# Performance work log

Hardware: AMD Instinct MI355X
Metric: run time of the kernel (lower is better)

## Reference

```python
import jax, jax.numpy as jnp
import numpy as np

NUM_CLASSES = 1000
MEM_SIZE = 200
FEAT_DIM = 512
BATCH = 512
TEMP = 0.07
MARGIN = 0.5
K_POS = 50   # memory positives per anchor (source: memory_positives[:50])
K_NEG = 20   # memory negatives per other class (source: [:20])


def _l2norm(x, axis=-1, eps=1e-12):
    n = jnp.sqrt(jnp.sum(x * x, axis=axis, keepdims=True))
    return x / jnp.maximum(n, eps)


def setup_inputs() -> dict:
    key = jax.random.key(0)
    k1, k2, k3 = jax.random.split(key, 3)
    features = jax.random.normal(k1, (BATCH, FEAT_DIM), dtype=jnp.float32)
    labels = jax.random.randint(k2, (BATCH,), 0, NUM_CLASSES, dtype=jnp.int32)
    memory_bank = jax.random.normal(k3, (NUM_CLASSES, MEM_SIZE, FEAT_DIM), dtype=jnp.float32)
    memory_bank = _l2norm(memory_bank, axis=2)  # buffer is normalized in __init__
    memory_ptr = jnp.zeros((NUM_CLASSES,), dtype=jnp.int32)
    return {"features": features, "labels": labels,
            "memory_bank": memory_bank, "memory_ptr": memory_ptr}


def reference(features, labels, memory_bank, memory_ptr):
    B, D = features.shape
    C, M, _ = memory_bank.shape

    f = _l2norm(features, axis=1)  # [B, D]

    # ---- memory-bank update (no_grad in torch): write each normalized feature
    # at ptr[label] + (rank of this sample among same-label samples in batch) ----
    onehot = jax.nn.one_hot(labels, C, dtype=jnp.int32)          # [B, C]
    cum = jnp.cumsum(onehot, axis=0)                              # [B, C]
    rank = cum[jnp.arange(B), labels] - 1                         # prior same-label count
    group_size = cum[-1][labels]                                  # occurrences of own label
    first_idx = jnp.argmax(onehot, axis=0)                        # first batch index per class
    write_pos = (memory_ptr[labels] + rank) % M
    mem = memory_bank.at[labels, write_pos].set(jax.lax.stop_gradient(f))
    mem = jax.lax.stop_gradient(mem)

    # ---- in-batch positives (faithful to the source's mask quirk:
    # positions compared against the FULL-batch first-occurrence index) ----
    S_batch = (f @ f.T) / TEMP                                    # [B, B]
    same = labels[:, None] == labels[None, :]
    batch_mask = same & (rank[None, :] != first_idx[labels][:, None]) & (group_size[:, None] > 1)
    pos_sum_batch = jnp.sum(jnp.where(batch_mask, S_batch, 0.0), axis=1)
    cnt_batch = jnp.sum(batch_mask, axis=1)

    # ---- memory similarities: only first K_POS slots are ever used ----
    S_mem = jnp.einsum('bd,ckd->bck', f, mem[:, :K_POS]) / TEMP   # [B, C, K_POS]

    # positives: own class, first K_POS slots
    own = S_mem[jnp.arange(B), labels]                            # [B, K_POS]
    pos_sum = pos_sum_batch + jnp.sum(own, axis=1)
    pos_cnt = (cnt_batch + K_POS).astype(f.dtype)
    pos_loss = -pos_sum / pos_cnt

    # negatives: all other classes, first K_NEG slots; hard-negative mean if any > margin
    sims_neg = S_mem[:, :, :K_NEG]                                # [B, C, K_NEG]
    cls_mask = (jnp.arange(C)[None, :] != labels[:, None])[:, :, None]
    hard = (sims_neg > MARGIN) & cls_mask
    hard_cnt = jnp.sum(hard, axis=(1, 2))
    hard_sum = jnp.sum(jnp.where(hard, sims_neg, 0.0), axis=(1, 2))
    all_sum = jnp.sum(jnp.where(cls_mask, sims_neg, 0.0), axis=(1, 2))
    all_cnt = jnp.asarray((C - 1) * K_NEG, dtype=f.dtype)
    neg_loss = jnp.where(hard_cnt > 0,
                         hard_sum / jnp.maximum(hard_cnt, 1).astype(f.dtype),
                         all_sum / all_cnt)

    return jnp.mean(pos_loss + neg_loss)
```

## Files before the change

kernel.cpp:

```cpp
#include <hip/hip_runtime.h>
#include <hip/hip_bf16.h>
#include <math.h>

#define BATCH 512
#define FEAT 512
#define NCLS 1000
#define MSZ 200
#define KP 50
#define KN 20
#define INV_TEMP (1.0f/0.07f)
#define MARGIN 0.5f
#define NBROWS 20032
#define NCB 313
#define NPART (NCB*2)

typedef __attribute__((ext_vector_type(8))) short short8;
typedef __attribute__((ext_vector_type(4))) float f32x4;

__device__ __forceinline__ unsigned short f2bf(float x) {
    __hip_bfloat16 h = __float2bfloat16(x);
    return *reinterpret_cast<unsigned short*>(&h);
}

__device__ __forceinline__ void gload_lds16(const void* g, void* l) {
    __builtin_amdgcn_global_load_lds(
        (const __attribute__((address_space(1))) void*)g,
        (__attribute__((address_space(3))) void*)l, 16, 0, 0);
}

__global__ void k_init(int* __restrict__ ov, float* __restrict__ own_sum) {
    int i = blockIdx.x * blockDim.x + threadIdx.x;
    if (i < NCLS * KP) ov[i] = -1;
    if (i < BATCH) own_sum[i] = 0.f;
}

__global__ void k_norm(const float* __restrict__ x, float* __restrict__ f,
                       unsigned short* __restrict__ fb) {
    int row = blockIdx.x;
    int t = threadIdx.x;
    float4 v = ((const float4*)(x + (size_t)row * FEAT))[t];
    float ss = v.x*v.x + v.y*v.y + v.z*v.z + v.w*v.w;
    for (int off = 32; off; off >>= 1) ss += __shfl_down(ss, off);
    __shared__ float w[2];
    if ((t & 63) == 0) w[t >> 6] = ss;
    __syncthreads();
    float inv = 1.f / fmaxf(sqrtf(w[0] + w[1]), 1e-12f);
    float4 o; o.x = v.x*inv; o.y = v.y*inv; o.z = v.z*inv; o.w = v.w*inv;
    ((float4*)(f + (size_t)row * FEAT))[t] = o;
    unsigned long long pk = (unsigned long long)f2bf(o.x)
                          | ((unsigned long long)f2bf(o.y) << 16)
                          | ((unsigned long long)f2bf(o.z) << 32)
                          | ((unsigned long long)f2bf(o.w) << 48);
    *(unsigned long long*)(fb + (size_t)row * FEAT + t * 4) = pk;
}

__global__ void k_meta(const int* __restrict__ labels, const int* __restrict__ mptr,
                       int* __restrict__ rank, int* __restrict__ gs,
                       int* __restrict__ fidx, int* __restrict__ ov) {
    __shared__ int lab[BATCH];
    int i = threadIdx.x;
    lab[i] = labels[i];
    __syncthreads();
    int l = lab[i];
    int r = 0, cnt = 0, first = -1;
    for (int j = 0; j < BATCH; j++) {
        if (lab[j] == l) { if (j < i) r++; cnt++; if (first < 0) first = j; }
    }
    rank[i] = r; gs[i] = cnt; fidx[i] = first;
    int wp = (mptr[l] + r) % MSZ;
    if (wp < KP) ov[l * KP + wp] = i;
}

__global__ __launch_bounds__(256) void k_conv(const float* __restrict__ f,
                                              const float* __restrict__ bank,
                                              const int* __restrict__ ov,
                                              unsigned short* __restrict__ Bm) {
    int g = blockIdx.x * 4 + (threadIdx.x >> 6);
    int lane = threadIdx.x & 63;
    unsigned short* dst = Bm + (size_t)g * FEAT + lane * 8;
    if (g >= NCLS * KN) {
        short8 z = {0,0,0,0,0,0,0,0};
        *(short8*)dst = z;
        return;
    }
    int c = g / KN, s = g - c * KN;
    int o = ov[c * KP + s];
    const float* src = (o >= 0) ? (f + (size_t)o * FEAT)
                                : (bank + ((size_t)c * MSZ + s) * FEAT);
    const float4* s4 = (const float4*)(src + lane * 8);
    float4 v0 = s4[0], v1 = s4[1];
    short8 out;
    out[0] = (short)f2bf(v0.x); out[1] = (short)f2bf(v0.y);
    out[2] = (short)f2bf(v0.z); out[3] = (short)f2bf(v0.w);
    out[4] = (short)f2bf(v1.x); out[5] = (short)f2bf(v1.y);
    out[6] = (short)f2bf(v1.z); out[7] = (short)f2bf(v1.w);
    *(short8*)dst = out;
}

__global__ void k_batchpos(const float* __restrict__ f, const int* __restrict__ labels,
                           const int* __restrict__ rank, const int* __restrict__ gs,
                           const int* __restrict__ fidx,
                           float* __restrict__ psb, float* __restrict__ cb) {
    int i = blockIdx.x;
    int t = threadIdx.x;
    __shared__ float fi[FEAT];
    for (int d = t; d < FEAT; d += 256) fi[d] = f[(size_t)i * FEAT + d];
    __syncthreads();
    int li = labels[i], fi_first = fidx[i], gsi = gs[i];
    float s = 0.f, c = 0.f;
    if (gsi > 1) {
        for (int j = t; j < BATCH; j += 256) {
            if (labels[j] == li && rank[j] != fi_first) {
                const float4* fj = (const float4*)(f + (size_t)j * FEAT);
                float acc = 0.f;
                #pragma unroll 8
                for (int d = 0; d < FEAT / 4; d++) {
                    float4 a = ((const float4*)fi)[d];
                    float4 b = fj[d];
                    acc += a.x*b.x + a.y*b.y + a.z*b.z + a.w*b.w;
                }
                s += acc * INV_TEMP;
                c += 1.f;
            }
        }
    }
    for (int off = 32; off; off >>= 1) { s += __shfl_down(s, off); c += __shfl_down(c, off); }
    __shared__ float ws[4], wc[4];
    if ((t & 63) == 0) { ws[t >> 6] = s; wc[t >> 6] = c; }
    __syncthreads();
    if (t == 0) {
        psb[i] = ws[0] + ws[1] + ws[2] + ws[3];
        cb[i]  = wc[0] + wc[1] + wc[2] + wc[3];
    }
}

#define BK 64
__global__ __launch_bounds__(256) void k_main(
    const unsigned short* __restrict__ fb, const unsigned short* __restrict__ Bm,
    const int* __restrict__ labels,
    float* __restrict__ own_sum,
    float* __restrict__ pa_all, float* __restrict__ pa_hs, float* __restrict__ pa_hc)
{
    int cb = blockIdx.y;
    int rbase = blockIdx.x * 128;
    int t = threadIdx.x;
    int w = t >> 6, lane = t & 63;
    int wr = w >> 1, wc = w & 1;
    int ln15 = lane & 15, quad = lane >> 4;

    __shared__ __align__(16) unsigned short As[128][BK];
    __shared__ __align__(16) unsigned short Bs[64][BK];

    f32x4 acc[4][2];
    #pragma unroll
    for (int i = 0; i < 4; i++)
        #pragma unroll
        for (int j = 0; j < 2; j++) acc[i][j] = (f32x4){0.f, 0.f, 0.f, 0.f};

    const char* aSrc[4]; void* aDst[4];
    const char* bSrc[2]; void* bDst[2];
    #pragma unroll
    for (int q = 0; q < 4; q++) {
        unsigned int L = q * 4096 + w * 1024 + lane * 16;
        int row = L >> 7;
        int part = L & 127;
        aSrc[q] = (const char*)fb + (size_t)(rbase + row) * (FEAT * 2) + part;
        aDst[q] = (char*)&As[0][0] + (q * 4096 + w * 1024);
    }
    #pragma unroll
    for (int q = 0; q < 2; q++) {
        unsigned int L = q * 4096 + w * 1024 + lane * 16;
        int row = L >> 7;
        int part = L & 127;
        bSrc[q] = (const char*)Bm + (size_t)(cb * 64 + row) * (FEAT * 2) + part;
        bDst[q] = (char*)&Bs[0][0] + (q * 4096 + w * 1024);
    }

    for (int k0 = 0; k0 < FEAT; k0 += BK) {
        __syncthreads();
        #pragma unroll
        for (int q = 0; q < 4; q++) gload_lds16(aSrc[q] + k0 * 2, aDst[q]);
        #pragma unroll
        for (int q = 0; q < 2; q++) gload_lds16(bSrc[q] + k0 * 2, bDst[q]);
        __syncthreads();

        #pragma unroll
        for (int kh = 0; kh < BK; kh += 32) {
            short8 a[4], b[2];
            #pragma unroll
            for (int i = 0; i < 4; i++)
                a[i] = *(const short8*)&As[wr * 64 + i * 16 + ln15][kh + quad * 8];
            #pragma unroll
            for (int j = 0; j < 2; j++)
                b[j] = *(const short8*)&Bs[wc * 32 + j * 16 + ln15][kh + quad * 8];
            #pragma unroll
            for (int i = 0; i < 4; i++)
                #pragma unroll
                for (int j = 0; j < 2; j++)
                    acc[i][j] = __builtin_amdgcn_mfma_f32_16x16x32_bf16(a[i], b[j], acc[i][j], 0, 0, 0);
        }
    }

    #pragma unroll
    for (int i = 0; i < 4; i++) {
        #pragma unroll
        for (int r = 0; r < 4; r++) {
            int grow = rbase + wr * 64 + i * 16 + quad * 4 + r;
            int lab = labels[grow];
            float own = 0.f, alls = 0.f, hs = 0.f, hc = 0.f;
            #pragma unroll
            for (int j = 0; j < 2; j++) {
                int gcol = cb * 64 + wc * 32 + j * 16 + ln15;
                float sim = acc[i][j][r] * INV_TEMP;
                if (gcol < NCLS * KN) {
                    int c = gcol / KN;
                    if (c == lab) {
                        own += sim;
                    } else {
                        alls += sim;
                        if (sim > MARGIN) { hs += sim; hc += 1.f; }
                    }
                }
            }
            #pragma unroll
            for (int off = 8; off; off >>= 1) {
                own  += __shfl_down(own,  off, 16);
                alls += __shfl_down(alls, off, 16);
                hs   += __shfl_down(hs,   off, 16);
                hc   += __shfl_down(hc,   off, 16);
            }
            if (ln15 == 0) {
                size_t pidx = (size_t)(cb * 2 + wc) * BATCH + grow;
                pa_all[pidx] = alls; pa_hs[pidx] = hs; pa_hc[pidx] = hc;
                if (own != 0.f) atomicAdd(&own_sum[grow], own);
            }
        }
    }
}

__global__ __launch_bounds__(256) void k_ownextra(
    const float* __restrict__ f, const float* __restrict__ bank,
    const int* __restrict__ labels, const int* __restrict__ ov,
    float* __restrict__ own2)
{
    int row = blockIdx.x;
    int t = threadIdx.x, w = t >> 6, lane = t & 63;
    int c = labels[row];
    float a0=0,a1=0,a2=0,a3=0,a4=0,a5=0,a6=0,a7=0;
    for (int s = KN + w; s < KP; s += 4) {
        int o = ov[c * KP + s];
        const float* src = (o >= 0) ? (f + (size_t)o * FEAT)
                                    : (bank + ((size_t)c * MSZ + s) * FEAT);
        const float4* s4 = (const float4*)(src + lane * 8);
        float4 v0 = s4[0], v1 = s4[1];
        a0 += v0.x; a1 += v0.y; a2 += v0.z; a3 += v0.w;
        a4 += v1.x; a5 += v1.y; a6 += v1.z; a7 += v1.w;
    }
    const float4* f4 = (const float4*)(f + (size_t)row * FEAT + lane * 8);
    float4 fa = f4[0], fbv = f4[1];
    float p = fa.x*a0 + fa.y*a1 + fa.z*a2 + fa.w*a3
            + fbv.x*a4 + fbv.y*a5 + fbv.z*a6 + fbv.w*a7;
    for (int off = 32; off; off >>= 1) p += __shfl_down(p, off);
    __shared__ float ws[4];
    if (lane == 0) ws[w] = p;
    __syncthreads();
    if (t == 0) own2[row] = (ws[0] + ws[1] + ws[2] + ws[3]) * INV_TEMP;
}

__global__ void k_reduce(const float* __restrict__ pa_all, const float* __restrict__ pa_hs,
                         const float* __restrict__ pa_hc,
                         float* __restrict__ all_sum, float* __restrict__ hard_sum,
                         float* __restrict__ hard_cnt)
{
    int row = blockIdx.x;
    int t = threadIdx.x;
    float a = 0.f, h = 0.f, hc = 0.f;
    for (int p = t; p < NPART; p += 256) {
        size_t idx = (size_t)p * BATCH + row;
        a += pa_all[idx]; h += pa_hs[idx]; hc += pa_hc[idx];
    }
    for (int off = 32; off; off >>= 1) {
        a += __shfl_down(a, off); h += __shfl_down(h, off); hc += __shfl_down(hc, off);
    }
    __shared__ float wa[4], wh[4], wcn[4];
    int w = t >> 6, lane = t & 63;
    if (lane == 0) { wa[w] = a; wh[w] = h; wcn[w] = hc; }
    __syncthreads();
    if (t == 0) {
        all_sum[row]  = wa[0] + wa[1] + wa[2] + wa[3];
        hard_sum[row] = wh[0] + wh[1] + wh[2] + wh[3];
        hard_cnt[row] = wcn[0] + wcn[1] + wcn[2] + wcn[3];
    }
}

__global__ void k_final(const float* __restrict__ own_sum, const float* __restrict__ own2,
                        const float* __restrict__ all_sum,
                        const float* __restrict__ hard_sum, const float* __restrict__ hard_cnt,
                        const float* __restrict__ psb, const float* __restrict__ cb,
                        float* __restrict__ out) {
    int i = threadIdx.x;
    float pos = -(psb[i] + own_sum[i] + own2[i]) / (cb[i] + (float)KP);
    float hcnt = hard_cnt[i];
    float neg = (hcnt > 0.f) ? hard_sum[i] / fmaxf(hcnt, 1.f)
                             : all_sum[i] / ((float)(NCLS - 1) * (float)KN);
    float v = pos + neg;
    for (int off = 32; off; off >>= 1) v += __shfl_down(v, off);
    __shared__ float w[8];
    if ((i & 63) == 0) w[i >> 6] = v;
    __syncthreads();
    if (i == 0) {
        float s = 0.f;
        for (int k = 0; k < 8; k++) s += w[k];
        out[0] = s / (float)BATCH;
    }
}

extern "C" void kernel_launch(void* const* d_in, const int* in_sizes, int n_in,
                              void* d_out, int out_size, void* d_ws, size_t ws_size,
                              hipStream_t stream) {
    const float* features = (const float*)d_in[0];
    const int*   labels   = (const int*)d_in[1];
    const float* bank     = (const float*)d_in[2];
    const int*   mptr     = (const int*)d_in[3];
    float* out = (float*)d_out;

    float* f            = (float*)d_ws;
    unsigned short* fb  = (unsigned short*)(f + BATCH * FEAT);
    unsigned short* Bm  = fb + (size_t)BATCH * FEAT;
    int*   ov           = (int*)(Bm + (size_t)NBROWS * FEAT);
    int*   rank         = ov + NCLS * KP;
    int*   gs           = rank + BATCH;
    int*   fidx         = gs + BATCH;
    float* own_sum      = (float*)(fidx + BATCH);
    float* own2         = own_sum + BATCH;
    float* all_sum      = own2 + BATCH;
    float* hard_sum     = all_sum + BATCH;
    float* hard_cnt     = hard_sum + BATCH;
    float* psb          = hard_cnt + BATCH;
    float* cb           = psb + BATCH;
    float* pa_all       = cb + BATCH;
    float* pa_hs        = pa_all + (size_t)NPART * BATCH;
    float* pa_hc        = pa_hs + (size_t)NPART * BATCH;

    k_init<<<(NCLS * KP + 255) / 256, 256, 0, stream>>>(ov, own_sum);
    k_norm<<<BATCH, 128, 0, stream>>>(features, f, fb);
    k_meta<<<1, BATCH, 0, stream>>>(labels, mptr, rank, gs, fidx, ov);
    k_conv<<<NBROWS / 4, 256, 0, stream>>>(f, bank, ov, Bm);
    k_batchpos<<<BATCH, 256, 0, stream>>>(f, labels, rank, gs, fidx, psb, cb);
    dim3 g5(BATCH / 128, NCB);
    k_main<<<g5, 256, 0, stream>>>(fb, Bm, labels, own_sum, pa_all, pa_hs, pa_hc);
    k_ownextra<<<BATCH, 256, 0, stream>>>(f, bank, labels, ov, own2);
    k_reduce<<<BATCH, 256, 0, stream>>>(pa_all, pa_hs, pa_hc, all_sum, hard_sum, hard_cnt);
    k_final<<<1, BATCH, 0, stream>>>(own_sum, own2, all_sum, hard_sum, hard_cnt, psb, cb, out);
}
```

Before: 548.9 us.

## Enlarge GEMM column tile, XOR-swizzle bf16 layout, and fuse small kernels

The main MFMA kernel's column tile grows from 64 to 128 memory rows per block, halving the grid and doubling B reuse per A load. Both bf16 operand buffers are stored with a per-row XOR chunk swizzle, so the LDS fragment reads avoid bank conflicts. The own-class extra-slot dot product is merged into the batch-positive kernel, and the reduce and final kernels become one tail kernel that accumulates the mean via atomicAdd. The changes cut launch count and LDS conflicts, at the cost of more accumulator registers and a nondeterministic float atomic for the final sum.

```diff
diff --git a/kernel.cpp b/kernel.cpp
--- a/kernel.cpp
+++ b/kernel.cpp
@@ -10,8 +10,8 @@
 #define KN 20
 #define INV_TEMP (1.0f/0.07f)
 #define MARGIN 0.5f
-#define NBROWS 20032
-#define NCB 313
+#define NBROWS 20096
+#define NCB 157
 #define NPART (NCB*2)
 
 typedef __attribute__((ext_vector_type(8))) short short8;
@@ -28,10 +28,12 @@
         (__attribute__((address_space(3))) void*)l, 16, 0, 0);
 }
 
-__global__ void k_init(int* __restrict__ ov, float* __restrict__ own_sum) {
+__global__ void k_init(int* __restrict__ ov, float* __restrict__ own_sum,
+                       float* __restrict__ out) {
     int i = blockIdx.x * blockDim.x + threadIdx.x;
     if (i < NCLS * KP) ov[i] = -1;
     if (i < BATCH) own_sum[i] = 0.f;
+    if (i == 0) out[0] = 0.f;
 }
 
 __global__ void k_norm(const float* __restrict__ x, float* __restrict__ f,
@@ -51,7 +53,11 @@
                           | ((unsigned long long)f2bf(o.y) << 16)
                           | ((unsigned long long)f2bf(o.z) << 32)
                           | ((unsigned long long)f2bf(o.w) << 48);
-    *(unsigned long long*)(fb + (size_t)row * FEAT + t * 4) = pk;
+    int group = t >> 4;
+    int chunk = (t >> 1) & 7;
+    int off8  = (t & 1) * 4;
+    int idx = group * 64 + ((chunk ^ (row & 7)) * 8) + off8;
+    *(unsigned long long*)(fb + (size_t)row * FEAT + idx) = pk;
 }
 
 __global__ void k_meta(const int* __restrict__ labels, const int* __restrict__ mptr,
@@ -77,7 +83,9 @@
                                               unsigned short* __restrict__ Bm) {
     int g = blockIdx.x * 4 + (threadIdx.x >> 6);
     int lane = threadIdx.x & 63;
-    unsigned short* dst = Bm + (size_t)g * FEAT + lane * 8;
+    int group = lane >> 3, chunk = lane & 7;
+    unsigned short* dst = Bm + (size_t)g * FEAT
+                        + group * 64 + ((chunk ^ (g & 7)) * 8);
     if (g >= NCLS * KN) {
         short8 z = {0,0,0,0,0,0,0,0};
         *(short8*)dst = z;
@@ -97,16 +105,20 @@
     *(short8*)dst = out;
 }
 
-__global__ void k_batchpos(const float* __restrict__ f, const int* __restrict__ labels,
-                           const int* __restrict__ rank, const int* __restrict__ gs,
-                           const int* __restrict__ fidx,
-                           float* __restrict__ psb, float* __restrict__ cb) {
+__global__ __launch_bounds__(256) void k_pos(
+    const float* __restrict__ f, const int* __restrict__ labels,
+    const int* __restrict__ rank, const int* __restrict__ gs,
+    const int* __restrict__ fidx, const int* __restrict__ ov,
+    const float* __restrict__ bank,
+    float* __restrict__ psb, float* __restrict__ cb, float* __restrict__ own2)
+{
     int i = blockIdx.x;
-    int t = threadIdx.x;
+    int t = threadIdx.x, w = t >> 6, lane = t & 63;
     __shared__ float fi[FEAT];
     for (int d = t; d < FEAT; d += 256) fi[d] = f[(size_t)i * FEAT + d];
     __syncthreads();
     int li = labels[i], fi_first = fidx[i], gsi = gs[i];
+
     float s = 0.f, c = 0.f;
     if (gsi > 1) {
         for (int j = t; j < BATCH; j += 256) {
@@ -124,13 +136,31 @@
             }
         }
     }
-    for (int off = 32; off; off >>= 1) { s += __shfl_down(s, off); c += __shfl_down(c, off); }
-    __shared__ float ws[4], wc[4];
-    if ((t & 63) == 0) { ws[t >> 6] = s; wc[t >> 6] = c; }
+    float a0=0,a1=0,a2=0,a3=0,a4=0,a5=0,a6=0,a7=0;
+    for (int sl = KN + w; sl < KP; sl += 4) {
+        int o = ov[li * KP + sl];
+        const float* src = (o >= 0) ? (f + (size_t)o * FEAT)
+                                    : (bank + ((size_t)li * MSZ + sl) * FEAT);
+        const float4* s4 = (const float4*)(src + lane * 8);
+        float4 v0 = s4[0], v1 = s4[1];
+        a0 += v0.x; a1 += v0.y; a2 += v0.z; a3 += v0.w;
+        a4 += v1.x; a5 += v1.y; a6 += v1.z; a7 += v1.w;
+    }
+    const float4* f4 = (const float4*)(fi + lane * 8);
+    float4 fa = f4[0], fbv = f4[1];
+    float p = fa.x*a0 + fa.y*a1 + fa.z*a2 + fa.w*a3
+            + fbv.x*a4 + fbv.y*a5 + fbv.z*a6 + fbv.w*a7;
+
+    for (int off = 32; off; off >>= 1) {
+        s += __shfl_down(s, off); c += __shfl_down(c, off); p += __shfl_down(p, off);
+    }
+    __shared__ float ws[4], wc[4], wp[4];
+    if (lane == 0) { ws[w] = s; wc[w] = c; wp[w] = p; }
     __syncthreads();
     if (t == 0) {
-        psb[i] = ws[0] + ws[1] + ws[2] + ws[3];
-        cb[i]  = wc[0] + wc[1] + wc[2] + wc[3];
+        psb[i]  = ws[0] + ws[1] + ws[2] + ws[3];
+        cb[i]   = wc[0] + wc[1] + wc[2] + wc[3];
+        own2[i] = (wp[0] + wp[1] + wp[2] + wp[3]) * INV_TEMP;
     }
 }
 
@@ -141,39 +171,33 @@
     float* __restrict__ own_sum,
     float* __restrict__ pa_all, float* __restrict__ pa_hs, float* __restrict__ pa_hc)
 {
-    int cb = blockIdx.y;
+    int cbk = blockIdx.y;
     int rbase = blockIdx.x * 128;
     int t = threadIdx.x;
     int w = t >> 6, lane = t & 63;
     int wr = w >> 1, wc = w & 1;
     int ln15 = lane & 15, quad = lane >> 4;
 
-    __shared__ __align__(16) unsigned short As[128][BK];
-    __shared__ __align__(16) unsigned short Bs[64][BK];
-
-    f32x4 acc[4][2];
+    __shared__ __align__(16) unsigned short As[128 * BK];
+    __shared__ __align__(16) unsigned short Bs[128 * BK];
+
+    f32x4 acc[4][4];
     #pragma unroll
     for (int i = 0; i < 4; i++)
         #pragma unroll
-        for (int j = 0; j < 2; j++) acc[i][j] = (f32x4){0.f, 0.f, 0.f, 0.f};
+        for (int j = 0; j < 4; j++) acc[i][j] = (f32x4){0.f, 0.f, 0.f, 0.f};
 
     const char* aSrc[4]; void* aDst[4];
-    const char* bSrc[2]; void* bDst[2];
+    const char* bSrc[4]; void* bDst[4];
     #pragma unroll
     for (int q = 0; q < 4; q++) {
         unsigned int L = q * 4096 + w * 1024 + lane * 16;
         int row = L >> 7;
         int part = L & 127;
         aSrc[q] = (const char*)fb + (size_t)(rbase + row) * (FEAT * 2) + part;
-        aDst[q] = (char*)&As[0][0] + (q * 4096 + w * 1024);
-    }
-    #pragma unroll
-    for (int q = 0; q < 2; q++) {
-        unsigned int L = q * 4096 + w * 1024 + lane * 16;
-        int row = L >> 7;
-        int part = L & 127;
-        bSrc[q] = (const char*)Bm + (size_t)(cb * 64 + row) * (FEAT * 2) + part;
-        bDst[q] = (char*)&Bs[0][0] + (q * 4096 + w * 1024);
+        aDst[q] = (char*)As + (q * 4096 + w * 1024);
+        bSrc[q] = (const char*)Bm + (size_t)(cbk * 128 + row) * (FEAT * 2) + part;
+        bDst[q] = (char*)Bs + (q * 4096 + w * 1024);
     }
 
     for (int k0 = 0; k0 < FEAT; k0 += BK) {
@@ -181,22 +205,27 @@
         #pragma unroll
         for (int q = 0; q < 4; q++) gload_lds16(aSrc[q] + k0 * 2, aDst[q]);
         #pragma unroll
-        for (int q = 0; q < 2; q++) gload_lds16(bSrc[q] + k0 * 2, bDst[q]);
+        for (int q = 0; q < 4; q++) gload_lds16(bSrc[q] + k0 * 2, bDst[q]);
         __syncthreads();
 
         #pragma unroll
         for (int kh = 0; kh < BK; kh += 32) {
-            short8 a[4], b[2];
-            #pragma unroll
-            for (int i = 0; i < 4; i++)
-                a[i] = *(const short8*)&As[wr * 64 + i * 16 + ln15][kh + quad * 8];
-            #pragma unroll
-            for (int j = 0; j < 2; j++)
-                b[j] = *(const short8*)&Bs[wc * 32 + j * 16 + ln15][kh + quad * 8];
+            int ch = (kh >> 3) + quad;
+            short8 a[4], b[4];
+            #pragma unroll
+            for (int i = 0; i < 4; i++) {
+                int ri = wr * 64 + i * 16 + ln15;
+                a[i] = *(const short8*)&As[ri * 64 + ((ch ^ (ri & 7)) * 8)];
+            }
+            #pragma unroll
+            for (int j = 0; j < 4; j++) {
+                int rj = wc * 64 + j * 16 + ln15;
+                b[j] = *(const short8*)&Bs[rj * 64 + ((ch ^ (rj & 7)) * 8)];
+            }
             #pragma unroll
             for (int i = 0; i < 4; i++)
                 #pragma unroll
-                for (int j = 0; j < 2; j++)
+                for (int j = 0; j < 4; j++)
                     acc[i][j] = __builtin_amdgcn_mfma_f32_16x16x32_bf16(a[i], b[j], acc[i][j], 0, 0, 0);
         }
     }
@@ -209,8 +238,8 @@
             int lab = labels[grow];
             float own = 0.f, alls = 0.f, hs = 0.f, hc = 0.f;
             #pragma unroll
-            for (int j = 0; j < 2; j++) {
-                int gcol = cb * 64 + wc * 32 + j * 16 + ln15;
+            for (int j = 0; j < 4; j++) {
+                int gcol = cbk * 128 + wc * 64 + j * 16 + ln15;
                 float sim = acc[i][j][r] * INV_TEMP;
                 if (gcol < NCLS * KN) {
                     int c = gcol / KN;
@@ -230,7 +259,7 @@
                 hc   += __shfl_down(hc,   off, 16);
             }
             if (ln15 == 0) {
-                size_t pidx = (size_t)(cb * 2 + wc) * BATCH + grow;
+                size_t pidx = (size_t)(cbk * 2 + wc) * BATCH + grow;
                 pa_all[pidx] = alls; pa_hs[pidx] = hs; pa_hc[pidx] = hc;
                 if (own != 0.f) atomicAdd(&own_sum[grow], own);
             }
@@ -238,39 +267,11 @@
     }
 }
 
-__global__ __launch_bounds__(256) void k_ownextra(
-    const float* __restrict__ f, const float* __restrict__ bank,
-    const int* __restrict__ labels, const int* __restrict__ ov,
-    float* __restrict__ own2)
-{
-    int row = blockIdx.x;
-    int t = threadIdx.x, w = t >> 6, lane = t & 63;
-    int c = labels[row];
-    float a0=0,a1=0,a2=0,a3=0,a4=0,a5=0,a6=0,a7=0;
-    for (int s = KN + w; s < KP; s += 4) {
-        int o = ov[c * KP + s];
-        const float* src = (o >= 0) ? (f + (size_t)o * FEAT)
-                                    : (bank + ((size_t)c * MSZ + s) * FEAT);
-        const float4* s4 = (const float4*)(src + lane * 8);
-        float4 v0 = s4[0], v1 = s4[1];
-        a0 += v0.x; a1 += v0.y; a2 += v0.z; a3 += v0.w;
-        a4 += v1.x; a5 += v1.y; a6 += v1.z; a7 += v1.w;
-    }
-    const float4* f4 = (const float4*)(f + (size_t)row * FEAT + lane * 8);
-    float4 fa = f4[0], fbv = f4[1];
-    float p = fa.x*a0 + fa.y*a1 + fa.z*a2 + fa.w*a3
-            + fbv.x*a4 + fbv.y*a5 + fbv.z*a6 + fbv.w*a7;
-    for (int off = 32; off; off >>= 1) p += __shfl_down(p, off);
-    __shared__ float ws[4];
-    if (lane == 0) ws[w] = p;
-    __syncthreads();
-    if (t == 0) own2[row] = (ws[0] + ws[1] + ws[2] + ws[3]) * INV_TEMP;
-}
-
-__global__ void k_reduce(const float* __restrict__ pa_all, const float* __restrict__ pa_hs,
-                         const float* __restrict__ pa_hc,
-                         float* __restrict__ all_sum, float* __restrict__ hard_sum,
-                         float* __restrict__ hard_cnt)
+__global__ void k_tail(const float* __restrict__ pa_all, const float* __restrict__ pa_hs,
+                       const float* __restrict__ pa_hc,
+                       const float* __restrict__ own_sum, const float* __restrict__ own2,
+                       const float* __restrict__ psb, const float* __restrict__ cb,
+                       float* __restrict__ out)
 {
     int row = blockIdx.x;
     int t = threadIdx.x;
@@ -287,31 +288,13 @@
     if (lane == 0) { wa[w] = a; wh[w] = h; wcn[w] = hc; }
     __syncthreads();
     if (t == 0) {
-        all_sum[row]  = wa[0] + wa[1] + wa[2] + wa[3];
-        hard_sum[row] = wh[0] + wh[1] + wh[2] + wh[3];
-        hard_cnt[row] = wcn[0] + wcn[1] + wcn[2] + wcn[3];
-    }
-}
-
-__global__ void k_final(const float* __restrict__ own_sum, const float* __restrict__ own2,
-                        const float* __restrict__ all_sum,
-                        const float* __restrict__ hard_sum, const float* __restrict__ hard_cnt,
-                        const float* __restrict__ psb, const float* __restrict__ cb,
-                        float* __restrict__ out) {
-    int i = threadIdx.x;
-    float pos = -(psb[i] + own_sum[i] + own2[i]) / (cb[i] + (float)KP);
-    float hcnt = hard_cnt[i];
-    float neg = (hcnt > 0.f) ? hard_sum[i] / fmaxf(hcnt, 1.f)
-                             : all_sum[i] / ((float)(NCLS - 1) * (float)KN);
-    float v = pos + neg;
-    for (int off = 32; off; off >>= 1) v += __shfl_down(v, off);
-    __shared__ float w[8];
-    if ((i & 63) == 0) w[i >> 6] = v;
-    __syncthreads();
-    if (i == 0) {
-        float s = 0.f;
-        for (int k = 0; k < 8; k++) s += w[k];
-        out[0] = s / (float)BATCH;
+        float alls = wa[0] + wa[1] + wa[2] + wa[3];
+        float hsum = wh[0] + wh[1] + wh[2] + wh[3];
+        float hcnt = wcn[0] + wcn[1] + wcn[2] + wcn[3];
+        float pos = -(psb[row] + own_sum[row] + own2[row]) / (cb[row] + (float)KP);
+        float neg = (hcnt > 0.f) ? hsum / fmaxf(hcnt, 1.f)
+                                 : alls / ((float)(NCLS - 1) * (float)KN);
+        atomicAdd(out, (pos + neg) * (1.f / (float)BATCH));
     }
 }
 
@@ -333,23 +316,18 @@
     int*   fidx         = gs + BATCH;
     float* own_sum      = (float*)(fidx + BATCH);
     float* own2         = own_sum + BATCH;
-    float* all_sum      = own2 + BATCH;
-    float* hard_sum     = all_sum + BATCH;
-    float* hard_cnt     = hard_sum + BATCH;
-    float* psb          = hard_cnt + BATCH;
+    float* psb          = own2 + BATCH;
     float* cb           = psb + BATCH;
     float* pa_all       = cb + BATCH;
     float* pa_hs        = pa_all + (size_t)NPART * BATCH;
     float* pa_hc        = pa_hs + (size_t)NPART * BATCH;
 
-    k_init<<<(NCLS * KP + 255) / 256, 256, 0, stream>>>(ov, own_sum);
+    k_init<<<(NCLS * KP + 255) / 256, 256, 0, stream>>>(ov, own_sum, out);
     k_norm<<<BATCH, 128, 0, stream>>>(features, f, fb);
     k_meta<<<1, BATCH, 0, stream>>>(labels, mptr, rank, gs, fidx, ov);
     k_conv<<<NBROWS / 4, 256, 0, stream>>>(f, bank, ov, Bm);
-    k_batchpos<<<BATCH, 256, 0, stream>>>(f, labels, rank, gs, fidx, psb, cb);
+    k_pos<<<BATCH, 256, 0, stream>>>(f, labels, rank, gs, fidx, ov, bank, psb, cb, own2);
     dim3 g5(BATCH / 128, NCB);
     k_main<<<g5, 256, 0, stream>>>(fb, Bm, labels, own_sum, pa_all, pa_hs, pa_hc);
-    k_ownextra<<<BATCH, 256, 0, stream>>>(f, bank, labels, ov, own2);
-    k_reduce<<<BATCH, 256, 0, stream>>>(pa_all, pa_hs, pa_hc, all_sum, hard_sum, hard_cnt);
-    k_final<<<1, BATCH, 0, stream>>>(own_sum, own2, all_sum, hard_sum, hard_cnt, psb, cb, out);
-}
+    k_tail<<<BATCH, 256, 0, stream>>>(pa_all, pa_hs, pa_hc, own_sum, own2, psb, cb, out);
+}
```

Result: no change. 552.0 us (+0.6%).
